# Kernel tuning notes

Measured on AMD Instinct MI355X. Metric: run time of the kernel, lower is better.

Reference implementation:

```python
import jax, jax.numpy as jnp
import numpy as np

N, M, B, L, D = 100000, 256, 8, 128, 64
COORD_MAX = 1024


def setup_inputs() -> dict:
    key = jax.random.key(0)
    ks = jax.random.split(key, 9)
    # batch ids sorted so the original loop's centroid_offset == column index
    clu_b = jnp.sort(jax.random.randint(ks[0], (N, 1), 0, B))
    cen_b = jnp.sort(jax.random.randint(ks[1], (M, 1), 0, B))
    clu_xyz = jax.random.randint(ks[2], (N, 3), 0, COORD_MAX)
    cen_xyz = jax.random.randint(ks[3], (M, 3), 0, COORD_MAX)
    return {
        "cluster_coords": jnp.concatenate([clu_b, clu_xyz], axis=1).astype(jnp.int32),
        "centroid_coords": jnp.concatenate([cen_b, cen_xyz], axis=1).astype(jnp.int32),
        "cluster_feats": jax.random.normal(ks[4], (N, L), jnp.float32),
        "centroid_feats": jax.random.normal(ks[5], (M, L), jnp.float32),
        "centroid_conf": jax.random.uniform(ks[6], (M, 1), jnp.float32),
        "W": jax.random.normal(ks[7], (L, D), jnp.float32) * 0.05,
        "b": jax.random.normal(ks[8], (D,), jnp.float32) * 0.05,
    }


def reference(cluster_coords, centroid_coords, cluster_feats, centroid_feats,
              centroid_conf, W, b):
    # pointwise Conv3d(k=1) == linear on features
    clu = cluster_feats @ W + b                      # [N, D]
    nrm = jnp.maximum(jnp.linalg.norm(clu, axis=1, keepdims=True), 1e-12)
    clu = clu / nrm                                  # F.normalize(p=2, dim=1)
    cen = centroid_conf * (centroid_feats @ W + b)   # [M, D]

    # same-batch mask replaces the python loop + scatter
    valid = cluster_coords[:, 0][:, None] == centroid_coords[:, 0][None, :]  # [N, M]

    # pairwise L2 distance on spatial coords via squared expansion (exact for small ints)
    cc = cluster_coords[:, 1:].astype(jnp.float32)   # [N, 3]
    ec = centroid_coords[:, 1:].astype(jnp.float32)  # [M, 3]
    d2 = (jnp.sum(cc * cc, axis=1)[:, None]
          + jnp.sum(ec * ec, axis=1)[None, :]
          - 2.0 * cc @ ec.T)
    dist = jnp.maximum(jnp.sqrt(jnp.maximum(d2, 0.0)), 0.1)  # clamp(min=0.1)

    logits = jnp.where(valid, -dist, -jnp.inf)
    attn = jax.nn.softmax(logits, axis=-1)           # per-row over same-batch centroids
    attn = jnp.where(valid, attn, 0.0)               # rows w/ no centroids -> 0 (matches zeros init)

    out = (clu @ cen.T) * attn                       # [N, M]
    return out
```

## Files before the change

### kernel.cpp

```cpp
#include <hip/hip_runtime.h>
#include <stdint.h>


#define NN 100000
#define MM 256
#define LL 128
#define DD 64
#define NTILES (NN / 16)

typedef float f32x4 __attribute__((ext_vector_type(4)));
typedef __bf16 bf16x8 __attribute__((ext_vector_type(8)));
typedef __fp16 fp16x2 __attribute__((ext_vector_type(2)));

union U16x8 { uint4 u; bf16x8 v; unsigned short s[8]; };
union UH2 { unsigned int u; fp16x2 h; };

static __device__ __forceinline__ unsigned short f2bf(float f) {
  union { float f; unsigned int i; } t; t.f = f;
  unsigned int x = t.i;
  x += 0x7fffu + ((x >> 16) & 1u);
  return (unsigned short)(x >> 16);
}

__global__ __launch_bounds__(256) void prep_kernel(
    const int* __restrict__ cen_coords,
    const float* __restrict__ cen_feats,
    const float* __restrict__ conf,
    const float* __restrict__ W,
    const float* __restrict__ bvec,
    unsigned short* __restrict__ cen_ws,
    unsigned short* __restrict__ wt_ws,
    float4* __restrict__ cmeta_ws)
{
  int tid = threadIdx.x;
  if (blockIdx.x < 16) {
    int m = blockIdx.x * 16 + (tid >> 4);
    int c = tid & 15;
    float a0 = 0.f, a1 = 0.f, a2 = 0.f, a3 = 0.f;
    for (int l = 0; l < LL; l++) {
      float f = cen_feats[m * LL + l];
      const float* wr = W + l * DD + c;
      a0 += f * wr[0];  a1 += f * wr[16];
      a2 += f * wr[32]; a3 += f * wr[48];
    }
    float cf = conf[m];
    cen_ws[m * DD + c +  0] = f2bf(cf * (a0 + bvec[c +  0]));
    cen_ws[m * DD + c + 16] = f2bf(cf * (a1 + bvec[c + 16]));
    cen_ws[m * DD + c + 32] = f2bf(cf * (a2 + bvec[c + 32]));
    cen_ws[m * DD + c + 48] = f2bf(cf * (a3 + bvec[c + 48]));
  } else {
    for (int i = tid; i < LL * DD; i += 256) {
      int l = i >> 6, d = i & 63;
      wt_ws[d * LL + l] = f2bf(W[l * DD + d]);
    }
    {
      int4 cc = ((const int4*)cen_coords)[tid];
      float4 f;
      f.x = (float)cc.y + 4096.0f * (float)cc.x;
      f.y = (float)cc.z;
      f.z = (float)cc.w;
      f.w = 0.0f;
      cmeta_ws[tid] = f;
    }
  }
}

__global__ __launch_bounds__(256, 8) void k1_gemm1(
    const float* __restrict__ feats,
    const float* __restrict__ bvec,
    const unsigned short* __restrict__ wt_ws,
    float* __restrict__ out)
{
  __shared__ __align__(16) unsigned short clu_s[4][16 * 72];

  int tid = threadIdx.x;
  int wave = tid >> 6, lane = tid & 63;
  int q = lane >> 4, c = lane & 15;
  int tile = blockIdx.x * 4 + wave;
  if (tile >= NTILES) return;

  f32x4 acc[4] = {{0,0,0,0},{0,0,0,0},{0,0,0,0},{0,0,0,0}};
  {
    const float4* fb = (const float4*)(feats + (size_t)(tile * 16 + c) * LL);
    const uint4* wb = (const uint4*)wt_ws;
#pragma unroll
    for (int ks = 0; ks < 4; ks++) {
      float4 f0 = fb[ks * 8 + q * 2];
      float4 f1 = fb[ks * 8 + q * 2 + 1];
      U16x8 a;
      a.v[0] = (__bf16)f0.x; a.v[1] = (__bf16)f0.y; a.v[2] = (__bf16)f0.z; a.v[3] = (__bf16)f0.w;
      a.v[4] = (__bf16)f1.x; a.v[5] = (__bf16)f1.y; a.v[6] = (__bf16)f1.z; a.v[7] = (__bf16)f1.w;
#pragma unroll
      for (int nt = 0; nt < 4; nt++) {
        U16x8 b; b.u = wb[(nt * 16 + c) * 16 + ks * 4 + q];
        acc[nt] = __builtin_amdgcn_mfma_f32_16x16x32_bf16(a.v, b.v, acc[nt], 0, 0, 0);
      }
    }
  }
#pragma unroll
  for (int nt = 0; nt < 4; nt++) {
    float bv = bvec[nt * 16 + c];
    acc[nt][0] += bv; acc[nt][1] += bv; acc[nt][2] += bv; acc[nt][3] += bv;
  }
  float inv_nrm[4];
#pragma unroll
  for (int r = 0; r < 4; r++) {
    float s = acc[0][r]*acc[0][r] + acc[1][r]*acc[1][r] + acc[2][r]*acc[2][r] + acc[3][r]*acc[3][r];
    s += __shfl_xor(s, 1); s += __shfl_xor(s, 2); s += __shfl_xor(s, 4); s += __shfl_xor(s, 8);
    inv_nrm[r] = 1.0f / fmaxf(sqrtf(s), 1e-12f);
  }
#pragma unroll
  for (int nt = 0; nt < 4; nt++)
#pragma unroll
    for (int r = 0; r < 4; r++) {
      union { __bf16 h; unsigned short s; } u;
      u.h = (__bf16)(acc[nt][r] * inv_nrm[r]);
      clu_s[wave][(q * 4 + r) * 72 + nt * 16 + c] = u.s;
    }

  __builtin_amdgcn_sched_barrier(0);

  const uint4* cb = (const uint4*)(clu_s[wave]);
  uint4 s0 = cb[(lane >> 2) * 9 + (lane & 3) * 2];
  uint4 s1 = cb[(lane >> 2) * 9 + (lane & 3) * 2 + 1];
  uint4* stash = (uint4*)((char*)out + (size_t)tile * 16384);
  stash[lane * 2]     = s0;
  stash[lane * 2 + 1] = s1;
}

__global__ __launch_bounds__(256, 6) void k2_attn(
    const int4* __restrict__ clu_coords4,
    const unsigned short* __restrict__ cen_ws,
    const float4* __restrict__ cmeta,
    float* __restrict__ out)
{
  int tid = threadIdx.x;
  int wave = tid >> 6, lane = tid & 63;
  int q = lane >> 4, c = lane & 15;
  int tile = blockIdx.x * 4 + wave;
  if (tile >= NTILES) return;

  const uint4* stash = (const uint4*)((const char*)out + (size_t)tile * 16384);
  U16x8 a0, a1;
  a0.u = stash[c * 8 + q];
  a1.u = stash[c * 8 + 4 + q];

  float rx[4], ry[4], rz[4];
#pragma unroll
  for (int r = 0; r < 4; r++) {
    int4 rm = clu_coords4[tile * 16 + q * 4 + r];
    rx[r] = (float)rm.y + 4096.0f * (float)rm.x;
    ry[r] = (float)rm.z;
    rz[r] = (float)rm.w;
  }

  float d2m[4] = {1e30f, 1e30f, 1e30f, 1e30f};
#pragma unroll 4
  for (int mt = 0; mt < 16; mt++) {
    float4 cm = cmeta[mt * 16 + c];
#pragma unroll
    for (int r = 0; r < 4; r++) {
      float dx = rx[r] - cm.x, dy = ry[r] - cm.y, dz = rz[r] - cm.z;
      d2m[r] = fminf(d2m[r], dx * dx + dy * dy + dz * dz);
    }
  }
  float dmv[4];
#pragma unroll
  for (int r = 0; r < 4; r++) {
    d2m[r] = fminf(d2m[r], __shfl_xor(d2m[r], 1));
    d2m[r] = fminf(d2m[r], __shfl_xor(d2m[r], 2));
    d2m[r] = fminf(d2m[r], __shfl_xor(d2m[r], 4));
    d2m[r] = fminf(d2m[r], __shfl_xor(d2m[r], 8));
    dmv[r] = fmaxf(sqrtf(d2m[r]), 0.1f);
  }

  uint2 ep[16];
  float rsum[4] = {0.f, 0.f, 0.f, 0.f};
#pragma unroll
  for (int mt = 0; mt < 16; mt++) {
    float4 cm = cmeta[mt * 16 + c];
    float e[4];
#pragma unroll
    for (int r = 0; r < 4; r++) {
      float dx = rx[r] - cm.x, dy = ry[r] - cm.y, dz = rz[r] - cm.z;
      float d = fmaxf(sqrtf(dx * dx + dy * dy + dz * dz), 0.1f);
      e[r] = __expf(dmv[r] - d);
      rsum[r] += e[r];
    }
    UH2 p0, p1;
    p0.h = __builtin_amdgcn_cvt_pkrtz(e[0], e[1]);
    p1.h = __builtin_amdgcn_cvt_pkrtz(e[2], e[3]);
    ep[mt].x = p0.u;
    ep[mt].y = p1.u;
  }
  float scale[4];
#pragma unroll
  for (int r = 0; r < 4; r++) {
    rsum[r] += __shfl_xor(rsum[r], 1);
    rsum[r] += __shfl_xor(rsum[r], 2);
    rsum[r] += __shfl_xor(rsum[r], 4);
    rsum[r] += __shfl_xor(rsum[r], 8);
    scale[r] = (d2m[r] < 4.0e6f) ? 1.0f / rsum[r] : 0.f;
  }

  const uint4* cenb = (const uint4*)cen_ws;
  float* ob = out + (size_t)(tile * 16 + q * 4) * MM + c;
#pragma unroll
  for (int mt = 0; mt < 16; mt++) {
    U16x8 b0, b1;
    b0.u = cenb[(mt * 16 + c) * 8 + q];
    b1.u = cenb[(mt * 16 + c) * 8 + 4 + q];
    f32x4 dacc = {0, 0, 0, 0};
    dacc = __builtin_amdgcn_mfma_f32_16x16x32_bf16(a0.v, b0.v, dacc, 0, 0, 0);
    dacc = __builtin_amdgcn_mfma_f32_16x16x32_bf16(a1.v, b1.v, dacc, 0, 0, 0);
    UH2 p0, p1; p0.u = ep[mt].x; p1.u = ep[mt].y;
    ob[0 * MM + mt * 16] = dacc[0] * ((float)p0.h[0] * scale[0]);
    ob[1 * MM + mt * 16] = dacc[1] * ((float)p0.h[1] * scale[1]);
    ob[2 * MM + mt * 16] = dacc[2] * ((float)p1.h[0] * scale[2]);
    ob[3 * MM + mt * 16] = dacc[3] * ((float)p1.h[1] * scale[3]);
  }
}

extern "C" void kernel_launch(void* const* d_in, const int* in_sizes, int n_in,
                              void* d_out, int out_size, void* d_ws, size_t ws_size,
                              hipStream_t stream) {
  const int* clu_coords = (const int*)d_in[0];
  const int* cen_coords = (const int*)d_in[1];
  const float* clu_feats = (const float*)d_in[2];
  const float* cen_feats = (const float*)d_in[3];
  const float* conf      = (const float*)d_in[4];
  const float* W         = (const float*)d_in[5];
  const float* bvec      = (const float*)d_in[6];
  float* out = (float*)d_out;

  char* ws = (char*)d_ws;
  unsigned short* cen_ws = (unsigned short*)ws;
  unsigned short* wt_ws  = (unsigned short*)(ws + 32768);
  float4* cmeta_ws       = (float4*)(ws + 32768 + 16384);

  prep_kernel<<<17, 256, 0, stream>>>(cen_coords, cen_feats, conf, W, bvec,
                                      cen_ws, wt_ws, cmeta_ws);
  int nblk = (NTILES + 3) / 4;
  k1_gemm1<<<nblk, 256, 0, stream>>>(clu_feats, bvec, wt_ws, out);
  k2_attn<<<nblk, 256, 0, stream>>>((const int4*)clu_coords, cen_ws, cmeta_ws, out);
}
```

Measured before the change: 210.6 us.

## Fuse GEMM1 and attention kernels into one, issuing feature loads early

Merges the normalized-projection GEMM kernel and the attention/output kernel into a single kernel. The normalized bf16 cluster rows now stay in LDS instead of being stashed to the output buffer and read back. Feature loads are issued at the start so their latency overlaps the distance and softmax computation. The cost is higher register pressure, with occupancy hinted down to 4 blocks, and the loss of one launch boundary.

```diff
diff --git a/kernel.cpp b/kernel.cpp
--- a/kernel.cpp
+++ b/kernel.cpp
@@ -65,10 +65,13 @@
   }
 }
 
-__global__ __launch_bounds__(256, 8) void k1_gemm1(
+__global__ __launch_bounds__(256, 4) void main_kernel(
+    const int4* __restrict__ clu_coords4,
     const float* __restrict__ feats,
     const float* __restrict__ bvec,
+    const unsigned short* __restrict__ cen_ws,
     const unsigned short* __restrict__ wt_ws,
+    const float4* __restrict__ cmeta,
     float* __restrict__ out)
 {
   __shared__ __align__(16) unsigned short clu_s[4][16 * 72];
@@ -79,72 +82,13 @@
   int tile = blockIdx.x * 4 + wave;
   if (tile >= NTILES) return;
 
-  f32x4 acc[4] = {{0,0,0,0},{0,0,0,0},{0,0,0,0},{0,0,0,0}};
-  {
-    const float4* fb = (const float4*)(feats + (size_t)(tile * 16 + c) * LL);
-    const uint4* wb = (const uint4*)wt_ws;
-#pragma unroll
-    for (int ks = 0; ks < 4; ks++) {
-      float4 f0 = fb[ks * 8 + q * 2];
-      float4 f1 = fb[ks * 8 + q * 2 + 1];
-      U16x8 a;
-      a.v[0] = (__bf16)f0.x; a.v[1] = (__bf16)f0.y; a.v[2] = (__bf16)f0.z; a.v[3] = (__bf16)f0.w;
-      a.v[4] = (__bf16)f1.x; a.v[5] = (__bf16)f1.y; a.v[6] = (__bf16)f1.z; a.v[7] = (__bf16)f1.w;
-#pragma unroll
-      for (int nt = 0; nt < 4; nt++) {
-        U16x8 b; b.u = wb[(nt * 16 + c) * 16 + ks * 4 + q];
-        acc[nt] = __builtin_amdgcn_mfma_f32_16x16x32_bf16(a.v, b.v, acc[nt], 0, 0, 0);
-      }
-    }
-  }
-#pragma unroll
-  for (int nt = 0; nt < 4; nt++) {
-    float bv = bvec[nt * 16 + c];
-    acc[nt][0] += bv; acc[nt][1] += bv; acc[nt][2] += bv; acc[nt][3] += bv;
-  }
-  float inv_nrm[4];
-#pragma unroll
-  for (int r = 0; r < 4; r++) {
-    float s = acc[0][r]*acc[0][r] + acc[1][r]*acc[1][r] + acc[2][r]*acc[2][r] + acc[3][r]*acc[3][r];
-    s += __shfl_xor(s, 1); s += __shfl_xor(s, 2); s += __shfl_xor(s, 4); s += __shfl_xor(s, 8);
-    inv_nrm[r] = 1.0f / fmaxf(sqrtf(s), 1e-12f);
-  }
-#pragma unroll
-  for (int nt = 0; nt < 4; nt++)
-#pragma unroll
-    for (int r = 0; r < 4; r++) {
-      union { __bf16 h; unsigned short s; } u;
-      u.h = (__bf16)(acc[nt][r] * inv_nrm[r]);
-      clu_s[wave][(q * 4 + r) * 72 + nt * 16 + c] = u.s;
-    }
-
-  __builtin_amdgcn_sched_barrier(0);
-
-  const uint4* cb = (const uint4*)(clu_s[wave]);
-  uint4 s0 = cb[(lane >> 2) * 9 + (lane & 3) * 2];
-  uint4 s1 = cb[(lane >> 2) * 9 + (lane & 3) * 2 + 1];
-  uint4* stash = (uint4*)((char*)out + (size_t)tile * 16384);
-  stash[lane * 2]     = s0;
-  stash[lane * 2 + 1] = s1;
-}
-
-__global__ __launch_bounds__(256, 6) void k2_attn(
-    const int4* __restrict__ clu_coords4,
-    const unsigned short* __restrict__ cen_ws,
-    const float4* __restrict__ cmeta,
-    float* __restrict__ out)
-{
-  int tid = threadIdx.x;
-  int wave = tid >> 6, lane = tid & 63;
-  int q = lane >> 4, c = lane & 15;
-  int tile = blockIdx.x * 4 + wave;
-  if (tile >= NTILES) return;
-
-  const uint4* stash = (const uint4*)((const char*)out + (size_t)tile * 16384);
-  U16x8 a0, a1;
-  a0.u = stash[c * 8 + q];
-  a1.u = stash[c * 8 + 4 + q];
-
+  const float4* fb = (const float4*)(feats + (size_t)(tile * 16 + c) * LL);
+  float4 ff[8];
+#pragma unroll
+  for (int ks = 0; ks < 4; ks++) {
+    ff[2 * ks]     = fb[ks * 8 + q * 2];
+    ff[2 * ks + 1] = fb[ks * 8 + q * 2 + 1];
+  }
   float rx[4], ry[4], rz[4];
 #pragma unroll
   for (int r = 0; r < 4; r++) {
@@ -193,15 +137,59 @@
     ep[mt].x = p0.u;
     ep[mt].y = p1.u;
   }
-  float scale[4];
+  float sc[4];
 #pragma unroll
   for (int r = 0; r < 4; r++) {
     rsum[r] += __shfl_xor(rsum[r], 1);
     rsum[r] += __shfl_xor(rsum[r], 2);
     rsum[r] += __shfl_xor(rsum[r], 4);
     rsum[r] += __shfl_xor(rsum[r], 8);
-    scale[r] = (d2m[r] < 4.0e6f) ? 1.0f / rsum[r] : 0.f;
-  }
+    sc[r] = (d2m[r] < 4.0e6f) ? 1.0f / rsum[r] : 0.f;
+  }
+
+  f32x4 acc[4] = {{0,0,0,0},{0,0,0,0},{0,0,0,0},{0,0,0,0}};
+  {
+    const uint4* wb = (const uint4*)wt_ws;
+#pragma unroll
+    for (int ks = 0; ks < 4; ks++) {
+      float4 f0 = ff[2 * ks], f1 = ff[2 * ks + 1];
+      U16x8 a;
+      a.v[0] = (__bf16)f0.x; a.v[1] = (__bf16)f0.y; a.v[2] = (__bf16)f0.z; a.v[3] = (__bf16)f0.w;
+      a.v[4] = (__bf16)f1.x; a.v[5] = (__bf16)f1.y; a.v[6] = (__bf16)f1.z; a.v[7] = (__bf16)f1.w;
+#pragma unroll
+      for (int nt = 0; nt < 4; nt++) {
+        U16x8 b; b.u = wb[(nt * 16 + c) * 16 + ks * 4 + q];
+        acc[nt] = __builtin_amdgcn_mfma_f32_16x16x32_bf16(a.v, b.v, acc[nt], 0, 0, 0);
+      }
+    }
+  }
+#pragma unroll
+  for (int nt = 0; nt < 4; nt++) {
+    float bv = bvec[nt * 16 + c];
+    acc[nt][0] += bv; acc[nt][1] += bv; acc[nt][2] += bv; acc[nt][3] += bv;
+  }
+  float inv_nrm[4];
+#pragma unroll
+  for (int r = 0; r < 4; r++) {
+    float s = acc[0][r]*acc[0][r] + acc[1][r]*acc[1][r] + acc[2][r]*acc[2][r] + acc[3][r]*acc[3][r];
+    s += __shfl_xor(s, 1); s += __shfl_xor(s, 2); s += __shfl_xor(s, 4); s += __shfl_xor(s, 8);
+    inv_nrm[r] = 1.0f / fmaxf(sqrtf(s), 1e-12f);
+  }
+#pragma unroll
+  for (int nt = 0; nt < 4; nt++)
+#pragma unroll
+    for (int r = 0; r < 4; r++) {
+      union { __bf16 h; unsigned short s; } u;
+      u.h = (__bf16)(acc[nt][r] * inv_nrm[r]);
+      clu_s[wave][(q * 4 + r) * 72 + nt * 16 + c] = u.s;
+    }
+
+  __builtin_amdgcn_sched_barrier(0);
+
+  const uint4* cb = (const uint4*)(clu_s[wave]);
+  U16x8 a0, a1;
+  a0.u = cb[c * 9 + q];
+  a1.u = cb[c * 9 + 4 + q];
 
   const uint4* cenb = (const uint4*)cen_ws;
   float* ob = out + (size_t)(tile * 16 + q * 4) * MM + c;
@@ -214,10 +202,10 @@
     dacc = __builtin_amdgcn_mfma_f32_16x16x32_bf16(a0.v, b0.v, dacc, 0, 0, 0);
     dacc = __builtin_amdgcn_mfma_f32_16x16x32_bf16(a1.v, b1.v, dacc, 0, 0, 0);
     UH2 p0, p1; p0.u = ep[mt].x; p1.u = ep[mt].y;
-    ob[0 * MM + mt * 16] = dacc[0] * ((float)p0.h[0] * scale[0]);
-    ob[1 * MM + mt * 16] = dacc[1] * ((float)p0.h[1] * scale[1]);
-    ob[2 * MM + mt * 16] = dacc[2] * ((float)p1.h[0] * scale[2]);
-    ob[3 * MM + mt * 16] = dacc[3] * ((float)p1.h[1] * scale[3]);
+    ob[0 * MM + mt * 16] = dacc[0] * ((float)p0.h[0] * sc[0]);
+    ob[1 * MM + mt * 16] = dacc[1] * ((float)p0.h[1] * sc[1]);
+    ob[2 * MM + mt * 16] = dacc[2] * ((float)p1.h[0] * sc[2]);
+    ob[3 * MM + mt * 16] = dacc[3] * ((float)p1.h[1] * sc[3]);
   }
 }
 
@@ -240,7 +228,6 @@
 
   prep_kernel<<<17, 256, 0, stream>>>(cen_coords, cen_feats, conf, W, bvec,
                                       cen_ws, wt_ws, cmeta_ws);
-  int nblk = (NTILES + 3) / 4;
-  k1_gemm1<<<nblk, 256, 0, stream>>>(clu_feats, bvec, wt_ws, out);
-  k2_attn<<<nblk, 256, 0, stream>>>((const int4*)clu_coords, cen_ws, cmeta_ws, out);
-}
+  main_kernel<<<(NTILES + 3) / 4, 256, 0, stream>>>(
+      (const int4*)clu_coords, clu_feats, bvec, cen_ws, wt_ws, cmeta_ws, out);
+}
```

Measured after the change: 209.0 us. Within noise of the previous version (-0.8%).
